# Kernel tuning notes

Measured on AMD Instinct MI355X. Metric: run time of the kernel, lower is better.

## Reference

```python
import jax, jax.numpy as jnp
import numpy as np

B, S, D, H = 2, 2048, 1024, 16
DK = D // H
SCALE = 1.0 / np.sqrt(DK).astype(np.float32)


def setup_inputs() -> dict:
    key = jax.random.key(0)
    ks = jax.random.split(key, 7)
    std = 1.0 / np.sqrt(D).astype(np.float32)
    return {
        "query": jax.random.normal(ks[0], (B, S, D), jnp.float32),
        "key": jax.random.normal(ks[1], (B, S, D), jnp.float32),
        "value": jax.random.normal(ks[2], (B, S, D), jnp.float32),
        "Wq": jax.random.normal(ks[3], (D, D), jnp.float32) * std,
        "Wk": jax.random.normal(ks[4], (D, D), jnp.float32) * std,
        "Wv": jax.random.normal(ks[5], (D, D), jnp.float32) * std,
        "Wo": jax.random.normal(ks[6], (D, D), jnp.float32) * std,
    }


def _split_heads(x):
    # [B, S, D] -> [B, H, S, DK]
    return x.reshape(B, S, H, DK).transpose(0, 2, 1, 3)


def reference(query, key, value, Wq, Wk, Wv, Wo):
    Q = _split_heads(query @ Wq)
    K = _split_heads(key @ Wk)
    V = _split_heads(value @ Wv)
    # explicit full-score attention, as in the original (mask=None, dropout off)
    scores = jnp.einsum("bhqd,bhkd->bhqk", Q, K) * SCALE
    attn = jax.nn.softmax(scores, axis=-1)
    out = jnp.einsum("bhqk,bhkd->bhqd", attn, V)
    out = out.transpose(0, 2, 1, 3).reshape(B, S, D)  # merge heads
    return out @ Wo
```

## Files before the change

kernel.cpp:

```cpp
#include <hip/hip_runtime.h>

#define B_ 2
#define S_ 2048
#define D_ 1024
#define H_ 16

typedef unsigned short u16;
typedef __bf16 bf16x8 __attribute__((ext_vector_type(8)));
typedef float f32x4 __attribute__((ext_vector_type(4)));
typedef unsigned short u16x8 __attribute__((ext_vector_type(8)));
typedef unsigned short u16x4 __attribute__((ext_vector_type(4)));

__device__ __forceinline__ unsigned swz128(unsigned o) {
  return o ^ (((o >> 7) & 7) << 4);
}

__device__ __forceinline__ void gload_lds16(const void* g, void* l) {
  __builtin_amdgcn_global_load_lds(
      (const __attribute__((address_space(1))) unsigned*)g,
      (__attribute__((address_space(3))) unsigned*)l, 16, 0, 0);
}

__device__ __forceinline__ u16 f2bf(float f) {
  union { float f; unsigned u; } v;
  v.f = f;
  unsigned u = v.u;
  return (u16)((u + 0x7fffu + ((u >> 16) & 1u)) >> 16);
}

struct C3 { const float* in[3]; u16* out[3]; };
__global__ __launch_bounds__(256) void cast3(C3 p, int n8) {
  int z = blockIdx.y;
  int i = blockIdx.x * 256 + threadIdx.x;
  if (i >= n8) return;
  const float4* src = (const float4*)p.in[z] + (size_t)i * 2;
  float4 a = src[0], b = src[1];
  u16x8 o;
  o[0] = f2bf(a.x); o[1] = f2bf(a.y); o[2] = f2bf(a.z); o[3] = f2bf(a.w);
  o[4] = f2bf(b.x); o[5] = f2bf(b.y); o[6] = f2bf(b.z); o[7] = f2bf(b.w);
  *((u16x8*)p.out[z] + i) = o;
}

struct T4 { const float* in[4]; u16* out[4]; };
__global__ __launch_bounds__(256) void transpose_w4(T4 p) {
  __shared__ u16 t[64][65];
  const float* in = p.in[blockIdx.z];
  u16* out = p.out[blockIdx.z];
  int r0 = blockIdx.y * 64, c0 = blockIdx.x * 64;
  for (int i = threadIdx.x; i < 4096; i += 256) {
    int r = i >> 6, c = i & 63;
    t[r][c] = f2bf(in[(size_t)(r0 + r) * 1024 + c0 + c]);
  }
  __syncthreads();
  for (int i = threadIdx.x; i < 4096; i += 256) {
    int r = i >> 6, c = i & 63;
    out[(size_t)(c0 + r) * 1024 + r0 + c] = t[c][r];
  }
}

__global__ __launch_bounds__(256) void transpose_v(const u16* __restrict__ V,
                                                   u16* __restrict__ VT) {
  __shared__ u16 t[64][65];
  int s0 = blockIdx.x * 64;
  int bh = blockIdx.y, b = bh >> 4, h = bh & 15;
  const u16* src = V + (size_t)b * S_ * D_ + h * 64;
  u16* dst = VT + (size_t)bh * 64 * S_;
  for (int i = threadIdx.x; i < 4096; i += 256) {
    int s = i >> 6, dk = i & 63;
    t[s][dk] = src[(size_t)(s0 + s) * D_ + dk];
  }
  __syncthreads();
  for (int i = threadIdx.x; i < 4096; i += 256) {
    int dk = i >> 6, s = i & 63;
    dst[(size_t)dk * S_ + s0 + s] = t[s][dk];
  }
}

template <bool OUTF32>
__device__ __forceinline__ void gemm_body(const u16* __restrict__ A,
                                          const u16* __restrict__ BT,
                                          void* __restrict__ Cv) {
  constexpr int K = 1024, N = 1024;
  __shared__ __align__(16) u16 lA[128 * 64];
  __shared__ __align__(16) u16 lB[64 * 64];
  const int tid = threadIdx.x, lane = tid & 63, w = tid >> 6;
  const int wr = w >> 1, wc = w & 1;
  const int m0 = blockIdx.x * 128, n0 = blockIdx.y * 64;
  const int g = lane >> 4, c16 = lane & 15;
  f32x4 acc[4][2] = {};
  const char* Ab = (const char*)(A + (size_t)m0 * K);
  const char* Bb = (const char*)(BT + (size_t)n0 * K);
  char* lAb = (char*)lA;
  char* lBb = (char*)lB;
  for (int kt = 0; kt < K; kt += 64) {
    for (int c = 0; c < 4; ++c) {
      unsigned o = w * 4096 + c * 1024 + lane * 16;
      unsigned u = swz128(o);
      gload_lds16(Ab + (size_t)(u >> 7) * (K * 2) + kt * 2 + (u & 127),
                  lAb + w * 4096 + c * 1024);
    }
    for (int c = 0; c < 2; ++c) {
      unsigned o = w * 2048 + c * 1024 + lane * 16;
      unsigned u = swz128(o);
      gload_lds16(Bb + (size_t)(u >> 7) * (K * 2) + kt * 2 + (u & 127),
                  lBb + w * 2048 + c * 1024);
    }
    asm volatile("s_waitcnt vmcnt(0)" ::: "memory");
    __syncthreads();
    for (int ks = 0; ks < 2; ++ks) {
      bf16x8 af[4], bf[2];
      for (int i = 0; i < 4; ++i) {
        unsigned row = wr * 64 + i * 16 + c16;
        unsigned o = row * 128 + ks * 64 + g * 16;
        af[i] = *(const bf16x8*)(lAb + (o ^ ((row & 7) << 4)));
      }
      for (int j = 0; j < 2; ++j) {
        unsigned row = wc * 32 + j * 16 + c16;
        unsigned o = row * 128 + ks * 64 + g * 16;
        bf[j] = *(const bf16x8*)(lBb + (o ^ ((row & 7) << 4)));
      }
      for (int i = 0; i < 4; ++i)
        for (int j = 0; j < 2; ++j)
          acc[i][j] = __builtin_amdgcn_mfma_f32_16x16x32_bf16(af[i], bf[j],
                                                              acc[i][j], 0, 0, 0);
    }
    __syncthreads();
  }
  for (int i = 0; i < 4; ++i)
    for (int j = 0; j < 2; ++j) {
      int row = m0 + wr * 64 + i * 16 + g * 4;
      int col = n0 + wc * 32 + j * 16 + c16;
      for (int r = 0; r < 4; ++r) {
        if constexpr (OUTF32)
          ((float*)Cv)[(size_t)(row + r) * N + col] = acc[i][j][r];
        else
          ((u16*)Cv)[(size_t)(row + r) * N + col] = f2bf(acc[i][j][r]);
      }
    }
}

struct G3 { const u16* A[3]; const u16* BT[3]; u16* C[3]; };
__global__ __launch_bounds__(256) void gemm_bt3(G3 p) {
  gemm_body<false>(p.A[blockIdx.z], p.BT[blockIdx.z], p.C[blockIdx.z]);
}
__global__ __launch_bounds__(256) void gemm_bt_f32(const u16* __restrict__ A,
                                                   const u16* __restrict__ BT,
                                                   float* __restrict__ C) {
  gemm_body<true>(A, BT, C);
}

__global__ __launch_bounds__(256) void flash_attn(const u16* __restrict__ Q,
                                                  const u16* __restrict__ K,
                                                  const u16* __restrict__ VT,
                                                  u16* __restrict__ O) {
  __shared__ __align__(16) u16 lP[64 * 64];
  __shared__ __align__(16) u16 lK[2][64 * 64];
  __shared__ __align__(16) u16 lV[2][64 * 64];
  const int tid = threadIdx.x, lane = tid & 63, w = tid >> 6;
  const int g = lane >> 4, c16 = lane & 15;
  const int q0 = blockIdx.x * 64;
  const int bh = blockIdx.y, b = bh >> 4, h = bh & 15;
  const char* Qb = (const char*)(Q + (size_t)(b * S_ + q0) * D_ + h * 64);
  const char* Kb = (const char*)(K + (size_t)b * S_ * D_ + h * 64);
  const char* Vb = (const char*)(VT + (size_t)bh * 64 * S_);
  char* lPb = (char*)lP;
  char* lKb = (char*)lK;
  char* lVb = (char*)lV;

  for (int c = 0; c < 2; ++c) {
    unsigned o = w * 2048 + c * 1024 + lane * 16;
    unsigned u = swz128(o);
    gload_lds16(Qb + (size_t)(u >> 7) * (D_ * 2) + (u & 127), lPb + w * 2048 + c * 1024);
    gload_lds16(Kb + (size_t)(u >> 7) * (D_ * 2) + (u & 127), lKb + w * 2048 + c * 1024);
    gload_lds16(Vb + (size_t)(u >> 7) * (S_ * 2) + (u & 127), lVb + w * 2048 + c * 1024);
  }
  float m_run = -INFINITY, l_run = 0.f;
  f32x4 oacc[4] = {};
  asm volatile("s_waitcnt vmcnt(0)" ::: "memory");
  __syncthreads();
  bf16x8 qf[2];
  {
    unsigned row = w * 16 + c16;
    for (int ks = 0; ks < 2; ++ks) {
      unsigned o = row * 128 + ks * 64 + g * 16;
      qf[ks] = *(const bf16x8*)(lPb + swz128(o));
    }
  }
  const float SC2 = 0.125f * 1.44269504088896340736f;
  int cur = 0;
  for (int kv0 = 0; kv0 < S_; kv0 += 64, cur ^= 1) {
    char* curK = lKb + cur * 8192;
    char* curV = lVb + cur * 8192;
    if (kv0 + 64 < S_) {
      char* nK = lKb + (cur ^ 1) * 8192;
      char* nV = lVb + (cur ^ 1) * 8192;
      for (int c = 0; c < 2; ++c) {
        unsigned o = w * 2048 + c * 1024 + lane * 16;
        unsigned u = swz128(o);
        gload_lds16(Kb + (size_t)(kv0 + 64 + (u >> 7)) * (D_ * 2) + (u & 127),
                    nK + w * 2048 + c * 1024);
        gload_lds16(Vb + (size_t)(u >> 7) * (S_ * 2) + (size_t)(kv0 + 64) * 2 + (u & 127),
                    nV + w * 2048 + c * 1024);
      }
    }
    f32x4 s[4] = {};
    for (int ks = 0; ks < 2; ++ks)
      for (int j = 0; j < 4; ++j) {
        unsigned row = j * 16 + c16;
        unsigned o = row * 128 + ks * 64 + g * 16;
        bf16x8 kf = *(const bf16x8*)(curK + swz128(o));
        s[j] = __builtin_amdgcn_mfma_f32_16x16x32_bf16(kf, qf[ks], s[j], 0, 0, 0);
      }
    float rm = s[0][0];
    for (int j = 0; j < 4; ++j)
      for (int r = 0; r < 4; ++r) rm = fmaxf(rm, s[j][r]);
    rm = fmaxf(rm, __shfl_xor(rm, 16));
    rm = fmaxf(rm, __shfl_xor(rm, 32));
    if (!__all((rm - m_run) * SC2 <= 8.0f)) {
      float mn = fmaxf(m_run, rm);
      float sc = exp2f((m_run - mn) * SC2);
      l_run *= sc;
      for (int i = 0; i < 4; ++i) oacc[i] *= sc;
      m_run = mn;
    }
    float rs = 0.f;
    unsigned qrow = w * 16 + c16;
    for (int j = 0; j < 4; ++j) {
      float p0 = exp2f((s[j][0] - m_run) * SC2);
      float p1 = exp2f((s[j][1] - m_run) * SC2);
      float p2 = exp2f((s[j][2] - m_run) * SC2);
      float p3 = exp2f((s[j][3] - m_run) * SC2);
      rs += (p0 + p1) + (p2 + p3);
      unsigned w0 = (unsigned)f2bf(p0) | ((unsigned)f2bf(p1) << 16);
      unsigned w1 = (unsigned)f2bf(p2) | ((unsigned)f2bf(p3) << 16);
      unsigned o = qrow * 128 + (unsigned)(j * 16 + g * 4) * 2;
      unsigned so = swz128(o);
      *(unsigned*)(lPb + so) = w0;
      *(unsigned*)(lPb + so + 4) = w1;
    }
    rs += __shfl_xor(rs, 16);
    rs += __shfl_xor(rs, 32);
    l_run += rs;
    for (int ks = 0; ks < 2; ++ks) {
      unsigned po = qrow * 128 + ks * 64 + g * 16;
      bf16x8 pf = *(const bf16x8*)(lPb + swz128(po));
      for (int i = 0; i < 4; ++i) {
        unsigned vo = (unsigned)(i * 16 + c16) * 128 + ks * 64 + g * 16;
        bf16x8 vf = *(const bf16x8*)(curV + swz128(vo));
        oacc[i] = __builtin_amdgcn_mfma_f32_16x16x32_bf16(vf, pf, oacc[i], 0, 0, 0);
      }
    }
    asm volatile("s_waitcnt vmcnt(0)" ::: "memory");
    __syncthreads();
  }
  float inv = 1.f / l_run;
  int q = q0 + w * 16 + c16;
  u16* orow = O + (size_t)(b * S_ + q) * D_ + h * 64;
  for (int i = 0; i < 4; ++i) {
    u16x4 ov;
    for (int r = 0; r < 4; ++r) ov[r] = f2bf(oacc[i][r] * inv);
    *(u16x4*)(orow + i * 16 + g * 4) = ov;
  }
}

extern "C" void kernel_launch(void* const* d_in, const int* in_sizes, int n_in,
                              void* d_out, int out_size, void* d_ws, size_t ws_size,
                              hipStream_t stream) {
  const float* q_in = (const float*)d_in[0];
  const float* k_in = (const float*)d_in[1];
  const float* v_in = (const float*)d_in[2];
  const float* Wq = (const float*)d_in[3];
  const float* Wk = (const float*)d_in[4];
  const float* Wv = (const float*)d_in[5];
  const float* Wo = (const float*)d_in[6];
  u16* ws = (u16*)d_ws;
  const size_t WSZ = (size_t)1024 * 1024;
  const size_t TSZ = (size_t)B_ * S_ * D_;
  u16* WqT = ws;
  u16* WkT = ws + WSZ;
  u16* WvT = ws + 2 * WSZ;
  u16* WoT = ws + 3 * WSZ;
  u16* Qc = ws + 4 * WSZ;
  u16* Kc = Qc + TSZ;
  u16* Vc = Kc + TSZ;
  u16* Qb = Vc + TSZ;
  u16* Kb = Qb + TSZ;
  u16* Vb = Kb + TSZ;
  u16* VTb = Kc;
  u16* Ob = Qc;
  dim3 tb(256);
  T4 tw = {{Wq, Wk, Wv, Wo}, {WqT, WkT, WvT, WoT}};
  transpose_w4<<<dim3(16, 16, 4), tb, 0, stream>>>(tw);
  int n8 = (int)(TSZ / 8);
  C3 cc = {{q_in, k_in, v_in}, {Qc, Kc, Vc}};
  cast3<<<dim3(n8 / 256, 3), tb, 0, stream>>>(cc, n8);
  G3 gg = {{Qc, Kc, Vc}, {WqT, WkT, WvT}, {Qb, Kb, Vb}};
  gemm_bt3<<<dim3(32, 16, 3), tb, 0, stream>>>(gg);
  transpose_v<<<dim3(32, 32), tb, 0, stream>>>(Vb, VTb);
  flash_attn<<<dim3(S_ / 64, B_ * H_), tb, 0, stream>>>(Qb, Kb, VTb, Ob);
  gemm_bt_f32<<<dim3(32, 16), tb, 0, stream>>>(Ob, WoT, (float*)d_out);
}
```

Baseline: 179.5 us.

## Fuse fp32-to-bf16 input cast into QKV GEMM and use packed bf16 conversions

Drops the separate cast kernel. The QKV projection GEMM now reads the fp32 activations directly, converts them to bf16 with v_cvt_pk_bf16_f32 in registers, and writes them into swizzled LDS. The QKV GEMM tile also grows from 128x64 to 128x128, which gives more MFMA work per block but launches half as many blocks and holds more accumulators per thread. The attention kernel swaps its manual bf16 rounding for the packed hardware conversion and uses 64-bit stores. The A operand now goes through synchronous register loads instead of async global-to-LDS loads, so latency is less hidden.

```diff
diff --git a/kernel.cpp b/kernel.cpp
--- a/kernel.cpp
+++ b/kernel.cpp
@@ -6,10 +6,11 @@
 #define H_ 16
 
 typedef unsigned short u16;
+typedef unsigned long long u64;
 typedef __bf16 bf16x8 __attribute__((ext_vector_type(8)));
 typedef float f32x4 __attribute__((ext_vector_type(4)));
 typedef unsigned short u16x8 __attribute__((ext_vector_type(8)));
-typedef unsigned short u16x4 __attribute__((ext_vector_type(4)));
+typedef unsigned uint4v __attribute__((ext_vector_type(4)));
 
 __device__ __forceinline__ unsigned swz128(unsigned o) {
   return o ^ (((o >> 7) & 7) << 4);
@@ -28,17 +29,10 @@
   return (u16)((u + 0x7fffu + ((u >> 16) & 1u)) >> 16);
 }
 
-struct C3 { const float* in[3]; u16* out[3]; };
-__global__ __launch_bounds__(256) void cast3(C3 p, int n8) {
-  int z = blockIdx.y;
-  int i = blockIdx.x * 256 + threadIdx.x;
-  if (i >= n8) return;
-  const float4* src = (const float4*)p.in[z] + (size_t)i * 2;
-  float4 a = src[0], b = src[1];
-  u16x8 o;
-  o[0] = f2bf(a.x); o[1] = f2bf(a.y); o[2] = f2bf(a.z); o[3] = f2bf(a.w);
-  o[4] = f2bf(b.x); o[5] = f2bf(b.y); o[6] = f2bf(b.z); o[7] = f2bf(b.w);
-  *((u16x8*)p.out[z] + i) = o;
+__device__ __forceinline__ unsigned cvtpk(float lo, float hi) {
+  unsigned d;
+  asm("v_cvt_pk_bf16_f32 %0, %1, %2" : "=v"(d) : "v"(lo), "v"(hi));
+  return d;
 }
 
 struct T4 { const float* in[4]; u16* out[4]; };
@@ -76,10 +70,74 @@
   }
 }
 
-template <bool OUTF32>
-__device__ __forceinline__ void gemm_body(const u16* __restrict__ A,
-                                          const u16* __restrict__ BT,
-                                          void* __restrict__ Cv) {
+struct QKV { const float* A[3]; const u16* BT[3]; u16* C[3]; };
+__global__ __launch_bounds__(256) void gemm_qkv(QKV p) {
+  constexpr int K = 1024, N = 1024;
+  __shared__ __align__(16) u16 lA[128 * 64];
+  __shared__ __align__(16) u16 lB[128 * 64];
+  const int tid = threadIdx.x, lane = tid & 63, w = tid >> 6;
+  const int wr = w >> 1, wc = w & 1;
+  const int m0 = blockIdx.x * 128, n0 = blockIdx.y * 128;
+  const int g = lane >> 4, c16 = lane & 15;
+  const int z = blockIdx.z;
+  f32x4 acc[4][4] = {};
+  const float* Af = p.A[z] + (size_t)m0 * K;
+  const char* Bb = (const char*)(p.BT[z] + (size_t)n0 * K);
+  u16* C = p.C[z];
+  char* lAb = (char*)lA;
+  char* lBb = (char*)lB;
+  for (int kt = 0; kt < K; kt += 64) {
+    for (int c = 0; c < 4; ++c) {
+      unsigned o = c * 4096 + tid * 16;
+      unsigned u = swz128(o);
+      gload_lds16(Bb + (size_t)(u >> 7) * (K * 2) + kt * 2 + (u & 127), lBb + o);
+    }
+    for (int c = 0; c < 4; ++c) {
+      unsigned o = c * 4096 + tid * 16;
+      unsigned row = o >> 7, kc = (o & 127) >> 1;
+      const float* s = Af + (size_t)row * K + kt + kc;
+      float4 f0 = *(const float4*)s;
+      float4 f1 = *(const float4*)(s + 4);
+      uint4v d;
+      d[0] = cvtpk(f0.x, f0.y);
+      d[1] = cvtpk(f0.z, f0.w);
+      d[2] = cvtpk(f1.x, f1.y);
+      d[3] = cvtpk(f1.z, f1.w);
+      *(uint4v*)(lAb + swz128(o)) = d;
+    }
+    asm volatile("s_waitcnt vmcnt(0)" ::: "memory");
+    __syncthreads();
+    for (int ks = 0; ks < 2; ++ks) {
+      bf16x8 af[4], bf[4];
+      for (int i = 0; i < 4; ++i) {
+        unsigned row = wr * 64 + i * 16 + c16;
+        unsigned o = row * 128 + ks * 64 + g * 16;
+        af[i] = *(const bf16x8*)(lAb + (o ^ ((row & 7) << 4)));
+      }
+      for (int j = 0; j < 4; ++j) {
+        unsigned row = wc * 64 + j * 16 + c16;
+        unsigned o = row * 128 + ks * 64 + g * 16;
+        bf[j] = *(const bf16x8*)(lBb + (o ^ ((row & 7) << 4)));
+      }
+      for (int i = 0; i < 4; ++i)
+        for (int j = 0; j < 4; ++j)
+          acc[i][j] = __builtin_amdgcn_mfma_f32_16x16x32_bf16(af[i], bf[j],
+                                                              acc[i][j], 0, 0, 0);
+    }
+    __syncthreads();
+  }
+  for (int i = 0; i < 4; ++i)
+    for (int j = 0; j < 4; ++j) {
+      int row = m0 + wr * 64 + i * 16 + g * 4;
+      int col = n0 + wc * 64 + j * 16 + c16;
+      for (int r = 0; r < 4; ++r)
+        C[(size_t)(row + r) * N + col] = f2bf(acc[i][j][r]);
+    }
+}
+
+__global__ __launch_bounds__(256) void gemm_bt_f32(const u16* __restrict__ A,
+                                                   const u16* __restrict__ BT,
+                                                   float* __restrict__ C) {
   constexpr int K = 1024, N = 1024;
   __shared__ __align__(16) u16 lA[128 * 64];
   __shared__ __align__(16) u16 lB[64 * 64];
@@ -130,23 +188,9 @@
     for (int j = 0; j < 2; ++j) {
       int row = m0 + wr * 64 + i * 16 + g * 4;
       int col = n0 + wc * 32 + j * 16 + c16;
-      for (int r = 0; r < 4; ++r) {
-        if constexpr (OUTF32)
-          ((float*)Cv)[(size_t)(row + r) * N + col] = acc[i][j][r];
-        else
-          ((u16*)Cv)[(size_t)(row + r) * N + col] = f2bf(acc[i][j][r]);
-      }
-    }
-}
-
-struct G3 { const u16* A[3]; const u16* BT[3]; u16* C[3]; };
-__global__ __launch_bounds__(256) void gemm_bt3(G3 p) {
-  gemm_body<false>(p.A[blockIdx.z], p.BT[blockIdx.z], p.C[blockIdx.z]);
-}
-__global__ __launch_bounds__(256) void gemm_bt_f32(const u16* __restrict__ A,
-                                                   const u16* __restrict__ BT,
-                                                   float* __restrict__ C) {
-  gemm_body<true>(A, BT, C);
+      for (int r = 0; r < 4; ++r)
+        C[(size_t)(row + r) * N + col] = acc[i][j][r];
+    }
 }
 
 __global__ __launch_bounds__(256) void flash_attn(const u16* __restrict__ Q,
@@ -231,12 +275,10 @@
       float p2 = exp2f((s[j][2] - m_run) * SC2);
       float p3 = exp2f((s[j][3] - m_run) * SC2);
       rs += (p0 + p1) + (p2 + p3);
-      unsigned w0 = (unsigned)f2bf(p0) | ((unsigned)f2bf(p1) << 16);
-      unsigned w1 = (unsigned)f2bf(p2) | ((unsigned)f2bf(p3) << 16);
+      unsigned w0 = cvtpk(p0, p1);
+      unsigned w1 = cvtpk(p2, p3);
       unsigned o = qrow * 128 + (unsigned)(j * 16 + g * 4) * 2;
-      unsigned so = swz128(o);
-      *(unsigned*)(lPb + so) = w0;
-      *(unsigned*)(lPb + so + 4) = w1;
+      *(u64*)(lPb + swz128(o)) = (u64)w0 | ((u64)w1 << 32);
     }
     rs += __shfl_xor(rs, 16);
     rs += __shfl_xor(rs, 32);
@@ -257,9 +299,9 @@
   int q = q0 + w * 16 + c16;
   u16* orow = O + (size_t)(b * S_ + q) * D_ + h * 64;
   for (int i = 0; i < 4; ++i) {
-    u16x4 ov;
-    for (int r = 0; r < 4; ++r) ov[r] = f2bf(oacc[i][r] * inv);
-    *(u16x4*)(orow + i * 16 + g * 4) = ov;
+    unsigned e0 = cvtpk(oacc[i][0] * inv, oacc[i][1] * inv);
+    unsigned e1 = cvtpk(oacc[i][2] * inv, oacc[i][3] * inv);
+    *(u64*)(orow + i * 16 + g * 4) = (u64)e0 | ((u64)e1 << 32);
   }
 }
 
@@ -280,22 +322,16 @@
   u16* WkT = ws + WSZ;
   u16* WvT = ws + 2 * WSZ;
   u16* WoT = ws + 3 * WSZ;
-  u16* Qc = ws + 4 * WSZ;
-  u16* Kc = Qc + TSZ;
-  u16* Vc = Kc + TSZ;
-  u16* Qb = Vc + TSZ;
+  u16* Qb = ws + 4 * WSZ;
   u16* Kb = Qb + TSZ;
   u16* Vb = Kb + TSZ;
-  u16* VTb = Kc;
-  u16* Ob = Qc;
+  u16* VTb = Vb + TSZ;
+  u16* Ob = VTb + TSZ;
   dim3 tb(256);
   T4 tw = {{Wq, Wk, Wv, Wo}, {WqT, WkT, WvT, WoT}};
   transpose_w4<<<dim3(16, 16, 4), tb, 0, stream>>>(tw);
-  int n8 = (int)(TSZ / 8);
-  C3 cc = {{q_in, k_in, v_in}, {Qc, Kc, Vc}};
-  cast3<<<dim3(n8 / 256, 3), tb, 0, stream>>>(cc, n8);
-  G3 gg = {{Qc, Kc, Vc}, {WqT, WkT, WvT}, {Qb, Kb, Vb}};
-  gemm_bt3<<<dim3(32, 16, 3), tb, 0, stream>>>(gg);
+  QKV gq = {{q_in, k_in, v_in}, {WqT, WkT, WvT}, {Qb, Kb, Vb}};
+  gemm_qkv<<<dim3(32, 8, 3), tb, 0, stream>>>(gq);
   transpose_v<<<dim3(32, 32), tb, 0, stream>>>(Vb, VTb);
   flash_attn<<<dim3(S_ / 64, B_ * H_), tb, 0, stream>>>(Qb, Kb, VTb, Ob);
   gemm_bt_f32<<<dim3(32, 16), tb, 0, stream>>>(Ob, WoT, (float*)d_out);
```

New measurement: 168.1 us. 6.3% less time.
